# Optimization experiments

Hardware: AMD Instinct MI355X
Metric: run time of the kernel (lower is better)

The kernel has to match this reference:

```python
import jax, jax.numpy as jnp
import numpy as np

B, L, D, H = 8, 512, 1024, 16
HD = D // H  # head dim = 64
SCALE = 1.0  # scale=False in __init__


def _rel_sinusoid(seq_len, dim):
    # RelativeSinusoidalPositionalEmbedding lookup for relative positions
    # arange(-L/2, L/2) (even L), sinusoid of the raw relative position.
    half = dim // 2
    inv = jnp.exp(jnp.arange(half, dtype=jnp.float32) * (-(np.log(10000.0) / (half - 1))))
    r = jnp.arange(-(seq_len // 2), seq_len // 2, dtype=jnp.float32)  # (L,)
    ang = r[:, None] * inv[None, :]  # (L, half)
    return jnp.concatenate([jnp.sin(ang), jnp.cos(ang)], axis=1)  # (L, dim)


def setup_inputs() -> dict:
    key = jax.random.key(0)
    ks = jax.random.split(key, 8)
    s = 0.02
    x = jax.random.normal(ks[0], (B, L, D), jnp.float32)
    mask = jax.random.randint(ks[1], (B, L), 0, 2).astype(jnp.int64)
    mask = mask.at[:, 0].set(1)  # ensure at least one valid key per row
    qmask = jax.random.randint(ks[2], (B, L), 0, 2).astype(jnp.int64)
    w_qkv = jax.random.normal(ks[3], (D, 3 * D), jnp.float32) * s
    w_qkpos = jax.random.normal(ks[4], (HD, 2 * D), jnp.float32) * s
    w_fc = jax.random.normal(ks[5], (D, D), jnp.float32) * s
    b_fc = jnp.zeros((D,), jnp.float32)
    shift = jnp.abs(jax.random.normal(ks[6], (1,), jnp.float32)) + 0.001
    bias = -jnp.abs(jax.random.normal(ks[7], (1,), jnp.float32))
    return dict(x=x, mask=mask, qmask=qmask, w_qkv=w_qkv, w_qkpos=w_qkpos,
                w_fc=w_fc, b_fc=b_fc, shift=shift, bias=bias)


def reference(x, mask, qmask, w_qkv, w_qkpos, w_fc, b_fc, shift, bias):
    # trans_type='self', use_Gaussian=True, dropout in eval mode (identity)
    b, l, d = x.shape
    qkv = x @ w_qkv  # (B, L, 3D)
    q, k, v = jnp.split(qkv, 3, axis=-1)
    q = q.reshape(b, l, H, HD).transpose(0, 2, 1, 3)  # (B,H,L,hd)
    k = k.reshape(b, l, H, HD).transpose(0, 2, 1, 3)
    v = v.reshape(b, l, H, HD).transpose(0, 2, 1, 3)

    pe = _rel_sinusoid(l, HD)               # (L, hd)
    y = pe @ w_qkpos                        # (L, 2D)
    q_p, k_p = jnp.split(y, 2, axis=-1)     # (L, D) each
    q_p = q_p.reshape(l, H, HD).transpose(1, 0, 2)  # (H, L, hd)
    k_p = k_p.reshape(l, H, HD).transpose(1, 0, 2)  # (H, L, hd)

    attn = jnp.einsum('bhid,bhjd->bhij', q, k) + jnp.einsum('hid,hjd->hij', q_p, k_p)[None]

    # speaker-identity masking: zero out cross-speaker scores (trans_type='self')
    qsame = qmask[:, :, None] == qmask[:, None, :]  # (B, L, L)
    attn = jnp.where(qsame[:, None], attn, 0.0)
    attn = attn / SCALE

    # key padding mask -> -inf
    attn = jnp.where(mask[:, None, None, :] == 0, -jnp.inf, attn)

    # Gaussian distance bias: -(shift * (i-j)^2 + bias)
    idx = jnp.arange(l, dtype=jnp.float32)
    sqd = (idx[:, None] - idx[None, :]) ** 2  # (L, L)
    attn = attn + (-(shift[0] * sqd + bias[0]))[None, None]

    attn = jax.nn.softmax(attn, axis=-1)
    out = jnp.einsum('bhij,bhjd->bhid', attn, v)  # (B,H,L,hd)
    out = out.transpose(0, 2, 1, 3).reshape(b, l, d)
    return out @ w_fc + b_fc
```

## Files before the change

kernel.cpp:

```cpp
#include <hip/hip_runtime.h>
#include <hip/hip_bf16.h>

#define BB 8
#define LL 512
#define DD 1024
#define HH 16
#define HD 64
#define LOG2E 1.4426950408889634f

typedef __attribute__((ext_vector_type(8))) unsigned short u16x8;
typedef __attribute__((ext_vector_type(4))) unsigned short u16x4;
typedef __attribute__((ext_vector_type(8))) __bf16 bf16x8;
typedef __attribute__((ext_vector_type(4))) float f32x4;
typedef __attribute__((ext_vector_type(16))) float f32x16;

#define DEV __device__ __forceinline__

DEV unsigned short f2bf(float f) {
    return __builtin_bit_cast(unsigned short, (__bf16)f);
}
DEV f32x4 mfma16(u16x8 a, u16x8 b, f32x4 c) {
    return __builtin_amdgcn_mfma_f32_16x16x32_bf16(
        __builtin_bit_cast(bf16x8, a), __builtin_bit_cast(bf16x8, b), c, 0, 0, 0);
}
DEV f32x16 mfma32(u16x8 a, u16x8 b, f32x16 c) {
    return __builtin_amdgcn_mfma_f32_32x32x16_bf16(
        __builtin_bit_cast(bf16x8, a), __builtin_bit_cast(bf16x8, b), c, 0, 0, 0);
}
typedef __attribute__((address_space(1))) void gv_t;
typedef __attribute__((address_space(3))) void lv_t;
DEV void gload16(const void* g, void* l) {
    __builtin_amdgcn_global_load_lds((gv_t*)g, (lv_t*)l, 16, 0, 0);
}


__global__ __launch_bounds__(256) void cvt_x(const float* __restrict__ in,
                                             unsigned short* __restrict__ out) {
    int i = blockIdx.x * 256 + threadIdx.x;
    f32x4 v = *(const f32x4*)(in + i * 4);
    u16x4 o;
    o[0] = f2bf(v[0]); o[1] = f2bf(v[1]); o[2] = f2bf(v[2]); o[3] = f2bf(v[3]);
    *(u16x4*)(out + i * 4) = o;
}

__global__ __launch_bounds__(256) void transpose_cvt(
    const float* __restrict__ in, unsigned short* __restrict__ out,
    int R, int C) {
    __shared__ unsigned short tile[32][33];
    int c0 = blockIdx.x * 32, r0 = blockIdx.y * 32;
    int tx = threadIdx.x & 31, ty = threadIdx.x >> 5;
#pragma unroll
    for (int i = 0; i < 32; i += 8)
        tile[ty + i][tx] = f2bf(in[(r0 + ty + i) * C + c0 + tx]);
    __syncthreads();
#pragma unroll
    for (int i = 0; i < 32; i += 8)
        out[(c0 + ty + i) * R + r0 + tx] = tile[tx][ty + i];
}

__global__ __launch_bounds__(256) void posg(
    const float* __restrict__ w, unsigned short* __restrict__ qpx,
    unsigned short* __restrict__ kpx) {
    __shared__ float peS[64][64];
    __shared__ float wS[64][32];
    int c0 = blockIdx.x * 32, i0 = blockIdx.y * 64;
    int t = threadIdx.x;
#pragma unroll
    for (int j = 0; j < 16; ++j) {
        int o = t + j * 256;
        int ri = o >> 6, d = o & 63, dd = d & 31;
        float inv = expf((float)dd * -0.2971077539347156f);
        float ang = (float)(i0 + ri - 256) * inv;
        peS[ri][d] = (d < 32) ? sinf(ang) : cosf(ang);
    }
#pragma unroll
    for (int j = 0; j < 8; ++j) {
        int o = t + j * 256;
        wS[o >> 5][o & 31] = w[(o >> 5) * 2048 + c0 + (o & 31)];
    }
    __syncthreads();
#pragma unroll
    for (int j = 0; j < 8; ++j) {
        int o = t + j * 256;
        int row = o >> 5, col = o & 31;
        float acc = 0.0f;
#pragma unroll
        for (int k = 0; k < 64; ++k) acc += peS[row][k] * wS[k][col];
        int c = c0 + col, i = i0 + row;
        int qt = i >> 5, lq = i & 31;
        int cc = (c < 1024) ? c : (c - 1024);
        int h = cc >> 6, kk = cc & 63;
        int ks = kk >> 4, h2 = (kk >> 3) & 1, jj = kk & 7;
        unsigned idx = ((unsigned)(h * 4096 + qt * 256 + ks * 64 + h2 * 32 + lq)
                        << 3) + jj;
        if (c < 1024) qpx[idx] = f2bf(acc * LOG2E);
        else          kpx[idx] = f2bf(acc);
    }
}

template <int MODE>
__global__ __launch_bounds__(256) void gemm_bt(
    const unsigned short* __restrict__ A, const unsigned short* __restrict__ Bt,
    int M, int N, int K, int NBX, unsigned short* __restrict__ o0,
    unsigned short* __restrict__ o1, unsigned short* __restrict__ o2,
    float* __restrict__ fout, const float* __restrict__ bias) {
    __shared__ __align__(16) unsigned short As[2][128 * 32];
    __shared__ __align__(16) unsigned short Bs[2][128 * 32];
    int g = blockIdx.x;
    int swz = (g & 7) * (gridDim.x >> 3) + (g >> 3);
    int bx = swz % NBX, by = swz / NBX;
    int m0 = by * 128, n0 = bx * 128;
    int t = threadIdx.x;
    int w = t >> 6, l = t & 63, lg = l >> 4, lc = l & 15;
    int wr = w >> 1, wc = w & 1;

    f32x4 acc[4][4] = {};

    int sr = t >> 2;
    int sc = (t & 3) ^ ((t >> 3) & 3);
    const unsigned short* Ab = A + (m0 + sr) * K + sc * 8;
    const unsigned short* Bb = Bt + (n0 + sr) * K + sc * 8;
    int rsw = (lc >> 1) & 3;

    auto stage = [&](int buf, int k0) {
        gload16(Ab + k0, &As[buf][w * 512]);
        gload16(Ab + 64 * K + k0, &As[buf][2048 + w * 512]);
        gload16(Bb + k0, &Bs[buf][w * 512]);
        gload16(Bb + 64 * K + k0, &Bs[buf][2048 + w * 512]);
    };

    stage(0, 0);
    stage(1, 32);
    int cur = 0;
    for (int k0 = 0; k0 < K; k0 += 32) {
        if (k0 + 32 < K)
            asm volatile("s_waitcnt vmcnt(4)" ::: "memory");
        else
            asm volatile("s_waitcnt vmcnt(0)" ::: "memory");
        __builtin_amdgcn_sched_barrier(0);
        __builtin_amdgcn_s_barrier();
        __builtin_amdgcn_sched_barrier(0);
        u16x8 af[4], bf[4];
#pragma unroll
        for (int mm = 0; mm < 4; ++mm)
            af[mm] = *(const u16x8*)&As[cur][(wr * 64 + mm * 16 + lc) * 32 +
                                             ((lg ^ rsw) << 3)];
#pragma unroll
        for (int nn = 0; nn < 4; ++nn)
            bf[nn] = *(const u16x8*)&Bs[cur][(wc * 64 + nn * 16 + lc) * 32 +
                                             ((lg ^ rsw) << 3)];
        asm volatile("s_waitcnt lgkmcnt(0)" ::: "memory");
        __builtin_amdgcn_sched_barrier(0);
        __builtin_amdgcn_s_barrier();
        __builtin_amdgcn_sched_barrier(0);
        if (k0 + 64 < K) stage(cur, k0 + 64);
#pragma unroll
        for (int mm = 0; mm < 4; ++mm)
#pragma unroll
            for (int nn = 0; nn < 4; ++nn)
                acc[mm][nn] = mfma16(af[mm], bf[nn], acc[mm][nn]);
        cur ^= 1;
    }

#pragma unroll
    for (int mm = 0; mm < 4; ++mm)
#pragma unroll
        for (int nn = 0; nn < 4; ++nn)
#pragma unroll
            for (int r = 0; r < 4; ++r) {
                int row = m0 + wr * 64 + mm * 16 + lg * 4 + r;
                int col = n0 + wc * 64 + nn * 16 + lc;
                float v = acc[mm][nn][r];
                if (MODE == 0) {
                    int bb = row >> 9, i = row & 511;
                    int which = col >> 10, dd = col & 1023;
                    int hh = dd >> 6, hd = dd & 63;
                    int bh2 = bb * HH + hh;
                    int tl = i >> 5, io = i & 31;
                    if (which == 2) {
                        int h2 = (io >> 2) & 1, ps = (io >> 4) & 1;
                        int j = (io & 3) | (((io >> 3) & 1) << 2);
                        int dblk = hd >> 5, lq = hd & 31;
                        unsigned idx = ((unsigned)(bh2 * 4096 + tl * 256 +
                                        (dblk * 2 + ps) * 64 + h2 * 32 + lq)
                                        << 3) + j;
                        o2[idx] = f2bf(v);
                    } else {
                        int ks = hd >> 4, h2 = (hd >> 3) & 1, j = hd & 7;
                        unsigned idx = ((unsigned)(bh2 * 4096 + tl * 256 +
                                        ks * 64 + h2 * 32 + io) << 3) + j;
                        if (which == 0) o0[idx] = f2bf(v * LOG2E);
                        else            o1[idx] = f2bf(v);
                    }
                } else {
                    fout[row * N + col] = v + bias[col];
                }
            }
}

__global__ __launch_bounds__(256, 1) void attn_k(
    const unsigned short* __restrict__ Qx, const unsigned short* __restrict__ Kx,
    const unsigned short* __restrict__ Vx, const unsigned short* __restrict__ QPx,
    const unsigned short* __restrict__ KPx, const int* __restrict__ mask,
    const int* __restrict__ qmask, const float* __restrict__ shp,
    unsigned short* __restrict__ out) {
    __shared__ float mbuf[2][2][64];
    __shared__ float lsbuf[2][2][64];
    __shared__ float obuf[2][2][64][33];

    int g = blockIdx.x;
    int bid = ((g & 7) << 6) + (g >> 3);
    int b = bid >> 6, h = (bid >> 2) & 15, qq = bid & 3;
    int t = threadIdx.x, w = t >> 6, l = t & 63;
    int qg = w & 1, kh = w >> 1;
    int lq = l & 31, hi = l >> 5;
    int c0 = qq * 4 + qg * 2;
    int qA = c0 * 32 + lq, qB = qA + 32;
    int bh = b * HH + h;

    const unsigned short* qbA  = Qx  + (((unsigned)(bh * 4096 + c0 * 256)) << 3) + (l << 3);
    const unsigned short* qpbA = QPx + (((unsigned)(h  * 4096 + c0 * 256)) << 3) + (l << 3);
    u16x8 qfA[4], pfA[4], qfB[4], pfB[4];
#pragma unroll
    for (int ks = 0; ks < 4; ++ks) {
        qfA[ks] = *(const u16x8*)(qbA + ks * 512);
        pfA[ks] = *(const u16x8*)(qpbA + ks * 512);
        qfB[ks] = *(const u16x8*)(qbA + 2048 + ks * 512);
        pfB[ks] = *(const u16x8*)(qpbA + 2048 + ks * 512);
    }

    unsigned long long km[4], qm[4];
#pragma unroll
    for (int t8 = 0; t8 < 4; ++t8) {
        int base = b * LL + (kh * 4 + t8) * 64 + l;
        km[t8] = __ballot(mask[base] != 0);
        qm[t8] = __ballot(qmask[base] != 0);
    }
    int qiA = (qmask[b * LL + qA] != 0) ? 1 : 0;
    int qiB = (qmask[b * LL + qB] != 0) ? 1 : 0;

    const float M0 = -1.0e30f, NEGF = -3.0e38f, THR = 8.0f;
    float negs = -(*shp) * LOG2E;
    float mA = M0, lsA = 0.0f, mB = M0, lsB = 0.0f;
    f32x16 oA0 = {}, oA1 = {}, oB0 = {}, oB1 = {};
    float fqA = (float)(qA - 4 * hi);
    float fqB = (float)(qB - 4 * hi);

#pragma unroll
    for (int tt = 0; tt < 8; ++tt) {
        int ttg = kh * 8 + tt;
        const unsigned short* kb  = Kx  + (((unsigned)(bh * 4096 + ttg * 256)) << 3) + (l << 3);
        const unsigned short* kpb = KPx + (((unsigned)(h  * 4096 + ttg * 256)) << 3) + (l << 3);
        const unsigned short* vb  = Vx  + (((unsigned)(bh * 4096 + ttg * 256)) << 3) + (l << 3);
        u16x8 kf[4], kpf[4], vf[4];
#pragma unroll
        for (int ks = 0; ks < 4; ++ks) {
            kf[ks]  = *(const u16x8*)(kb + ks * 512);
            kpf[ks] = *(const u16x8*)(kpb + ks * 512);
            vf[ks]  = *(const u16x8*)(vb + ks * 512);
        }
        f32x16 sA = {}, sB = {};
#pragma unroll
        for (int ks = 0; ks < 4; ++ks) {
            sA = mfma32(kf[ks], qfA[ks], sA);
            sB = mfma32(kf[ks], qfB[ks], sB);
        }
#pragma unroll
        for (int ks = 0; ks < 4; ++ks) {
            sA = mfma32(kpf[ks], pfA[ks], sA);
            sB = mfma32(kpf[ks], pfB[ks], sB);
        }

        unsigned kwn = ((unsigned)(km[tt >> 1] >> ((tt & 1) * 32))) >> (hi * 4);
        unsigned qwn = ((unsigned)(qm[tt >> 1] >> ((tt & 1) * 32))) >> (hi * 4);
        float btA = fqA - 32.0f * (float)ttg;
        float btB = fqB - 32.0f * (float)ttg;

        {
            float p[16];
#pragma unroll
            for (int r = 0; r < 16; ++r) {
                const int off = (r & 3) + 8 * (r >> 2);
                float v = sA[r];
                v = (((qwn >> off) & 1u) == (unsigned)qiA) ? v : 0.0f;
                float dr = btA - (float)off;
                v = __builtin_fmaf(negs * dr, dr, v);
                v = ((kwn >> off) & 1u) ? v : NEGF;
                p[r] = v;
            }
            float a0 = fmaxf(fmaxf(p[0], p[1]), fmaxf(p[2], p[3]));
            float a1 = fmaxf(fmaxf(p[4], p[5]), fmaxf(p[6], p[7]));
            float a2 = fmaxf(fmaxf(p[8], p[9]), fmaxf(p[10], p[11]));
            float a3 = fmaxf(fmaxf(p[12], p[13]), fmaxf(p[14], p[15]));
            float pmax = fmaxf(fmaxf(a0, a1), fmaxf(a2, a3));
            pmax = fmaxf(pmax, __shfl_xor(pmax, 32));
            if (!__all(pmax <= mA + THR)) {
                float mn = fmaxf(mA, pmax);
                float sc = __builtin_amdgcn_exp2f(mA - mn);
#pragma unroll
                for (int r = 0; r < 16; ++r) { oA0[r] *= sc; oA1[r] *= sc; }
                lsA *= sc;
                mA = mn;
            }
#pragma unroll
            for (int r = 0; r < 16; ++r) p[r] = __builtin_amdgcn_exp2f(p[r] - mA);
            lsA += (((p[0] + p[1]) + (p[2] + p[3])) + ((p[4] + p[5]) + (p[6] + p[7]))) +
                   (((p[8] + p[9]) + (p[10] + p[11])) +
                    ((p[12] + p[13]) + (p[14] + p[15])));
            u16x8 pf0, pf1;
#pragma unroll
            for (int j = 0; j < 8; ++j) { pf0[j] = f2bf(p[j]); pf1[j] = f2bf(p[8 + j]); }
            oA0 = mfma32(vf[0], pf0, oA0);
            oA0 = mfma32(vf[1], pf1, oA0);
            oA1 = mfma32(vf[2], pf0, oA1);
            oA1 = mfma32(vf[3], pf1, oA1);
        }
        {
            float p[16];
#pragma unroll
            for (int r = 0; r < 16; ++r) {
                const int off = (r & 3) + 8 * (r >> 2);
                float v = sB[r];
                v = (((qwn >> off) & 1u) == (unsigned)qiB) ? v : 0.0f;
                float dr = btB - (float)off;
                v = __builtin_fmaf(negs * dr, dr, v);
                v = ((kwn >> off) & 1u) ? v : NEGF;
                p[r] = v;
            }
            float a0 = fmaxf(fmaxf(p[0], p[1]), fmaxf(p[2], p[3]));
            float a1 = fmaxf(fmaxf(p[4], p[5]), fmaxf(p[6], p[7]));
            float a2 = fmaxf(fmaxf(p[8], p[9]), fmaxf(p[10], p[11]));
            float a3 = fmaxf(fmaxf(p[12], p[13]), fmaxf(p[14], p[15]));
            float pmax = fmaxf(fmaxf(a0, a1), fmaxf(a2, a3));
            pmax = fmaxf(pmax, __shfl_xor(pmax, 32));
            if (!__all(pmax <= mB + THR)) {
                float mn = fmaxf(mB, pmax);
                float sc = __builtin_amdgcn_exp2f(mB - mn);
#pragma unroll
                for (int r = 0; r < 16; ++r) { oB0[r] *= sc; oB1[r] *= sc; }
                lsB *= sc;
                mB = mn;
            }
#pragma unroll
            for (int r = 0; r < 16; ++r) p[r] = __builtin_amdgcn_exp2f(p[r] - mB);
            lsB += (((p[0] + p[1]) + (p[2] + p[3])) + ((p[4] + p[5]) + (p[6] + p[7]))) +
                   (((p[8] + p[9]) + (p[10] + p[11])) +
                    ((p[12] + p[13]) + (p[14] + p[15])));
            u16x8 pf0, pf1;
#pragma unroll
            for (int j = 0; j < 8; ++j) { pf0[j] = f2bf(p[j]); pf1[j] = f2bf(p[8 + j]); }
            oB0 = mfma32(vf[0], pf0, oB0);
            oB0 = mfma32(vf[1], pf1, oB0);
            oB1 = mfma32(vf[2], pf0, oB1);
            oB1 = mfma32(vf[3], pf1, oB1);
        }
    }

    if (kh == 1) {
        mbuf[qg][0][l] = mA;  lsbuf[qg][0][l] = lsA;
        mbuf[qg][1][l] = mB;  lsbuf[qg][1][l] = lsB;
#pragma unroll
        for (int r = 0; r < 16; ++r) {
            obuf[qg][0][l][r] = oA0[r];
            obuf[qg][0][l][16 + r] = oA1[r];
            obuf[qg][1][l][r] = oB0[r];
            obuf[qg][1][l][16 + r] = oB1[r];
        }
    }
    __syncthreads();
    if (kh == 0) {
        {
            float m1 = mbuf[qg][0][l], ls1 = lsbuf[qg][0][l];
            float mm = fmaxf(mA, m1);
            float sc0 = __builtin_amdgcn_exp2f(mA - mm);
            float sc1 = __builtin_amdgcn_exp2f(m1 - mm);
            float lsm = lsA * sc0 + ls1 * sc1;
            float rs = lsm + __shfl_xor(lsm, 32);
            float rinv = __builtin_amdgcn_rcpf(rs);
            unsigned short* ob = out + ((long)(b * LL + qA)) * DD + h * HD + hi * 4;
#pragma unroll
            for (int rg = 0; rg < 4; ++rg) {
                u16x4 pk0, pk1;
#pragma unroll
                for (int rr = 0; rr < 4; ++rr) {
                    int i = rg * 4 + rr;
                    float v0 = __builtin_fmaf(oA0[i], sc0, obuf[qg][0][l][i] * sc1);
                    float v1 = __builtin_fmaf(oA1[i], sc0, obuf[qg][0][l][16 + i] * sc1);
                    pk0[rr] = f2bf(v0 * rinv);
                    pk1[rr] = f2bf(v1 * rinv);
                }
                *(u16x4*)(ob + rg * 8) = pk0;
                *(u16x4*)(ob + 32 + rg * 8) = pk1;
            }
        }
        {
            float m1 = mbuf[qg][1][l], ls1 = lsbuf[qg][1][l];
            float mm = fmaxf(mB, m1);
            float sc0 = __builtin_amdgcn_exp2f(mB - mm);
            float sc1 = __builtin_amdgcn_exp2f(m1 - mm);
            float lsm = lsB * sc0 + ls1 * sc1;
            float rs = lsm + __shfl_xor(lsm, 32);
            float rinv = __builtin_amdgcn_rcpf(rs);
            unsigned short* ob = out + ((long)(b * LL + qB)) * DD + h * HD + hi * 4;
#pragma unroll
            for (int rg = 0; rg < 4; ++rg) {
                u16x4 pk0, pk1;
#pragma unroll
                for (int rr = 0; rr < 4; ++rr) {
                    int i = rg * 4 + rr;
                    float v0 = __builtin_fmaf(oB0[i], sc0, obuf[qg][1][l][i] * sc1);
                    float v1 = __builtin_fmaf(oB1[i], sc0, obuf[qg][1][l][16 + i] * sc1);
                    pk0[rr] = f2bf(v0 * rinv);
                    pk1[rr] = f2bf(v1 * rinv);
                }
                *(u16x4*)(ob + rg * 8) = pk0;
                *(u16x4*)(ob + 32 + rg * 8) = pk1;
            }
        }
    }
}

extern "C" void kernel_launch(void* const* d_in, const int* in_sizes, int n_in,
                              void* d_out, int out_size, void* d_ws,
                              size_t ws_size, hipStream_t stream) {
    const float* x     = (const float*)d_in[0];
    const int*   mask  = (const int*)d_in[1];
    const int*   qmask = (const int*)d_in[2];
    const float* w_qkv = (const float*)d_in[3];
    const float* w_qkp = (const float*)d_in[4];
    const float* w_fc  = (const float*)d_in[5];
    const float* b_fc  = (const float*)d_in[6];
    const float* shift = (const float*)d_in[7];

    char* ws = (char*)d_ws;
    unsigned short* xb   = (unsigned short*)(ws);
    unsigned short* qb   = (unsigned short*)(ws + 8388608);
    unsigned short* kb   = (unsigned short*)(ws + 16777216);
    unsigned short* vtb  = (unsigned short*)(ws + 25165824);
    unsigned short* qp   = (unsigned short*)(ws + 33554432);
    unsigned short* kp   = (unsigned short*)(ws + 34603008);
    unsigned short* wqt  = (unsigned short*)(ws + 35651584);
    unsigned short* wft  = (unsigned short*)(ws + 41943040);
    unsigned short* aout = (unsigned short*)(ws + 44040192);

    cvt_x<<<4096, 256, 0, stream>>>(x, xb);
    transpose_cvt<<<dim3(96, 32), 256, 0, stream>>>(w_qkv, wqt, 1024, 3072);
    transpose_cvt<<<dim3(32, 32), 256, 0, stream>>>(w_fc, wft, 1024, 1024);
    posg<<<dim3(64, 8), 256, 0, stream>>>(w_qkp, qp, kp);
    gemm_bt<0><<<768, 256, 0, stream>>>(xb, wqt, 4096, 3072, 1024, 24, qb, kb,
                                        vtb, nullptr, nullptr);
    attn_k<<<512, 256, 0, stream>>>(qb, kb, vtb, qp, kp, mask, qmask, shift,
                                    aout);
    gemm_bt<1><<<256, 256, 0, stream>>>(aout, wft, 4096, 1024, 1024, 8, nullptr,
                                        nullptr, nullptr, (float*)d_out, b_fc);
}
```

Measured before the change: 137.9 us.

## Merge prep kernels into one launch and triple-buffer GEMM LDS staging

```diff
diff --git a/kernel.cpp b/kernel.cpp
--- a/kernel.cpp
+++ b/kernel.cpp
@@ -34,67 +34,82 @@
 }
 
 
-__global__ __launch_bounds__(256) void cvt_x(const float* __restrict__ in,
-                                             unsigned short* __restrict__ out) {
-    int i = blockIdx.x * 256 + threadIdx.x;
-    f32x4 v = *(const f32x4*)(in + i * 4);
-    u16x4 o;
-    o[0] = f2bf(v[0]); o[1] = f2bf(v[1]); o[2] = f2bf(v[2]); o[3] = f2bf(v[3]);
-    *(u16x4*)(out + i * 4) = o;
-}
-
-__global__ __launch_bounds__(256) void transpose_cvt(
-    const float* __restrict__ in, unsigned short* __restrict__ out,
-    int R, int C) {
-    __shared__ unsigned short tile[32][33];
-    int c0 = blockIdx.x * 32, r0 = blockIdx.y * 32;
-    int tx = threadIdx.x & 31, ty = threadIdx.x >> 5;
-#pragma unroll
-    for (int i = 0; i < 32; i += 8)
-        tile[ty + i][tx] = f2bf(in[(r0 + ty + i) * C + c0 + tx]);
-    __syncthreads();
-#pragma unroll
-    for (int i = 0; i < 32; i += 8)
-        out[(c0 + ty + i) * R + r0 + tx] = tile[tx][ty + i];
-}
-
-__global__ __launch_bounds__(256) void posg(
-    const float* __restrict__ w, unsigned short* __restrict__ qpx,
+__global__ __launch_bounds__(256) void prep(
+    const float* __restrict__ x, unsigned short* __restrict__ xb,
+    const float* __restrict__ w_qkv, unsigned short* __restrict__ wqt,
+    const float* __restrict__ w_fc, unsigned short* __restrict__ wft,
+    const float* __restrict__ w_qkp, unsigned short* __restrict__ qpx,
     unsigned short* __restrict__ kpx) {
-    __shared__ float peS[64][64];
-    __shared__ float wS[64][32];
-    int c0 = blockIdx.x * 32, i0 = blockIdx.y * 64;
+    __shared__ __align__(16) char lds[24576];
+    int blk = blockIdx.x;
     int t = threadIdx.x;
-#pragma unroll
-    for (int j = 0; j < 16; ++j) {
-        int o = t + j * 256;
-        int ri = o >> 6, d = o & 63, dd = d & 31;
-        float inv = expf((float)dd * -0.2971077539347156f);
-        float ang = (float)(i0 + ri - 256) * inv;
-        peS[ri][d] = (d < 32) ? sinf(ang) : cosf(ang);
-    }
-#pragma unroll
-    for (int j = 0; j < 8; ++j) {
-        int o = t + j * 256;
-        wS[o >> 5][o & 31] = w[(o >> 5) * 2048 + c0 + (o & 31)];
-    }
-    __syncthreads();
-#pragma unroll
-    for (int j = 0; j < 8; ++j) {
-        int o = t + j * 256;
-        int row = o >> 5, col = o & 31;
-        float acc = 0.0f;
-#pragma unroll
-        for (int k = 0; k < 64; ++k) acc += peS[row][k] * wS[k][col];
-        int c = c0 + col, i = i0 + row;
-        int qt = i >> 5, lq = i & 31;
-        int cc = (c < 1024) ? c : (c - 1024);
-        int h = cc >> 6, kk = cc & 63;
-        int ks = kk >> 4, h2 = (kk >> 3) & 1, jj = kk & 7;
-        unsigned idx = ((unsigned)(h * 4096 + qt * 256 + ks * 64 + h2 * 32 + lq)
-                        << 3) + jj;
-        if (c < 1024) qpx[idx] = f2bf(acc * LOG2E);
-        else          kpx[idx] = f2bf(acc);
+    if (blk < 4096) {
+        int i = blk * 256 + t;
+        f32x4 v = *(const f32x4*)(x + i * 4);
+        u16x4 o;
+        o[0] = f2bf(v[0]); o[1] = f2bf(v[1]);
+        o[2] = f2bf(v[2]); o[3] = f2bf(v[3]);
+        *(u16x4*)(xb + i * 4) = o;
+    } else if (blk < 7168) {
+        int r = blk - 4096;
+        int c0 = (r % 96) * 32, r0 = (r / 96) * 32;
+        auto tile = (unsigned short(*)[33])lds;
+        int tx = t & 31, ty = t >> 5;
+#pragma unroll
+        for (int i = 0; i < 32; i += 8)
+            tile[ty + i][tx] = f2bf(w_qkv[(r0 + ty + i) * 3072 + c0 + tx]);
+        __syncthreads();
+#pragma unroll
+        for (int i = 0; i < 32; i += 8)
+            wqt[(c0 + ty + i) * 1024 + r0 + tx] = tile[tx][ty + i];
+    } else if (blk < 8192) {
+        int r = blk - 7168;
+        int c0 = (r % 32) * 32, r0 = (r / 32) * 32;
+        auto tile = (unsigned short(*)[33])lds;
+        int tx = t & 31, ty = t >> 5;
+#pragma unroll
+        for (int i = 0; i < 32; i += 8)
+            tile[ty + i][tx] = f2bf(w_fc[(r0 + ty + i) * 1024 + c0 + tx]);
+        __syncthreads();
+#pragma unroll
+        for (int i = 0; i < 32; i += 8)
+            wft[(c0 + ty + i) * 1024 + r0 + tx] = tile[tx][ty + i];
+    } else {
+        int r = blk - 8192;
+        int c0 = (r % 64) * 32, i0 = (r / 64) * 64;
+        auto peS = (float(*)[64])lds;
+        auto wS = (float(*)[32])(lds + 16384);
+#pragma unroll
+        for (int j = 0; j < 16; ++j) {
+            int o = t + j * 256;
+            int ri = o >> 6, d = o & 63, dd = d & 31;
+            float inv = expf((float)dd * -0.2971077539347156f);
+            float ang = (float)(i0 + ri - 256) * inv;
+            peS[ri][d] = (d < 32) ? sinf(ang) : cosf(ang);
+        }
+#pragma unroll
+        for (int j = 0; j < 8; ++j) {
+            int o = t + j * 256;
+            wS[o >> 5][o & 31] = w_qkp[(o >> 5) * 2048 + c0 + (o & 31)];
+        }
+        __syncthreads();
+#pragma unroll
+        for (int j = 0; j < 8; ++j) {
+            int o = t + j * 256;
+            int row = o >> 5, col = o & 31;
+            float acc = 0.0f;
+#pragma unroll
+            for (int k = 0; k < 64; ++k) acc += peS[row][k] * wS[k][col];
+            int c = c0 + col, i = i0 + row;
+            int qt = i >> 5, lq = i & 31;
+            int cc = (c < 1024) ? c : (c - 1024);
+            int h = cc >> 6, kk = cc & 63;
+            int ks = kk >> 4, h2 = (kk >> 3) & 1, jj = kk & 7;
+            unsigned idx = ((unsigned)(h * 4096 + qt * 256 + ks * 64 +
+                            h2 * 32 + lq) << 3) + jj;
+            if (c < 1024) qpx[idx] = f2bf(acc * LOG2E);
+            else          kpx[idx] = f2bf(acc);
+        }
     }
 }
 
@@ -104,8 +119,8 @@
     int M, int N, int K, int NBX, unsigned short* __restrict__ o0,
     unsigned short* __restrict__ o1, unsigned short* __restrict__ o2,
     float* __restrict__ fout, const float* __restrict__ bias) {
-    __shared__ __align__(16) unsigned short As[2][128 * 32];
-    __shared__ __align__(16) unsigned short Bs[2][128 * 32];
+    __shared__ __align__(16) unsigned short As[3][128 * 32];
+    __shared__ __align__(16) unsigned short Bs[3][128 * 32];
     int g = blockIdx.x;
     int swz = (g & 7) * (gridDim.x >> 3) + (g >> 3);
     int bx = swz % NBX, by = swz / NBX;
@@ -131,9 +146,13 @@
 
     stage(0, 0);
     stage(1, 32);
+    stage(2, 64);
     int cur = 0;
     for (int k0 = 0; k0 < K; k0 += 32) {
-        if (k0 + 32 < K)
+        int rem = (K - k0) >> 5;
+        if (rem > 2)
+            asm volatile("s_waitcnt vmcnt(8)" ::: "memory");
+        else if (rem == 2)
             asm volatile("s_waitcnt vmcnt(4)" ::: "memory");
         else
             asm volatile("s_waitcnt vmcnt(0)" ::: "memory");
@@ -153,13 +172,13 @@
         __builtin_amdgcn_sched_barrier(0);
         __builtin_amdgcn_s_barrier();
         __builtin_amdgcn_sched_barrier(0);
-        if (k0 + 64 < K) stage(cur, k0 + 64);
+        if (k0 + 96 < K) stage(cur, k0 + 96);
 #pragma unroll
         for (int mm = 0; mm < 4; ++mm)
 #pragma unroll
             for (int nn = 0; nn < 4; ++nn)
                 acc[mm][nn] = mfma16(af[mm], bf[nn], acc[mm][nn]);
-        cur ^= 1;
+        cur = (cur == 2) ? 0 : cur + 1;
     }
 
 #pragma unroll
@@ -443,10 +462,7 @@
     unsigned short* wft  = (unsigned short*)(ws + 41943040);
     unsigned short* aout = (unsigned short*)(ws + 44040192);
 
-    cvt_x<<<4096, 256, 0, stream>>>(x, xb);
-    transpose_cvt<<<dim3(96, 32), 256, 0, stream>>>(w_qkv, wqt, 1024, 3072);
-    transpose_cvt<<<dim3(32, 32), 256, 0, stream>>>(w_fc, wft, 1024, 1024);
-    posg<<<dim3(64, 8), 256, 0, stream>>>(w_qkp, qp, kp);
+    prep<<<8704, 256, 0, stream>>>(x, xb, w_qkv, wqt, w_fc, wft, w_qkp, qp, kp);
     gemm_bt<0><<<768, 256, 0, stream>>>(xb, wqt, 4096, 3072, 1024, 24, qb, kb,
                                         vtb, nullptr, nullptr);
     attn_k<<<512, 256, 0, stream>>>(qb, kb, vtb, qp, kp, mask, qmask, shift,
```

Measured after the change: 133.6 us. 3.2% less time.
